# Performance work log

Measured on AMD Instinct MI355X. Metric: run time of the kernel, lower is better.

## Reference

```python
import jax, jax.numpy as jnp
import numpy as np

B, S, HIDDEN = 1, 2048, 2048
NUM_HEADS, MLA_DIM = 16, 128
HEAD_DIM = HIDDEN // NUM_HEADS
ROPE_BASE = 10000.0


def setup_inputs() -> dict:
    key = jax.random.key(0)
    ks = jax.random.split(key, 5)
    sd = 0.02
    hidden_states = jax.random.normal(ks[0], (B, S, HIDDEN), dtype=jnp.float32)
    wq = jax.random.normal(ks[1], (HIDDEN, NUM_HEADS * MLA_DIM), dtype=jnp.float32) * sd
    wk = jax.random.normal(ks[2], (HIDDEN, NUM_HEADS * MLA_DIM), dtype=jnp.float32) * sd
    wv = jax.random.normal(ks[3], (HIDDEN, HIDDEN), dtype=jnp.float32) * sd
    wo = jax.random.normal(ks[4], (HIDDEN, HIDDEN), dtype=jnp.float32) * sd
    # causal additive mask [B, 1, S, S]
    causal = jnp.tril(jnp.ones((S, S), dtype=bool))
    attention_mask = jnp.where(causal, 0.0, -1e9).astype(jnp.float32)[None, None]
    attention_mask = jnp.broadcast_to(attention_mask, (B, 1, S, S))
    return {"hidden_states": hidden_states, "wq": wq, "wk": wk, "wv": wv,
            "wo": wo, "attention_mask": attention_mask}


def _rope_cos_sin(seq_len, dim, dtype):
    inv_freq = 1.0 / (ROPE_BASE ** (jnp.arange(0, dim, 2, dtype=jnp.float32) / dim))
    t = jnp.arange(seq_len, dtype=jnp.float32)
    freqs = jnp.einsum('i,j->ij', t, inv_freq)           # [S, dim/2]
    emb = jnp.concatenate([freqs, freqs], axis=-1)       # [S, dim]
    cos = jnp.cos(emb)[None, :, None, :].astype(dtype)   # [1, S, 1, dim]
    sin = jnp.sin(emb)[None, :, None, :].astype(dtype)
    return cos, sin


def _rotate_half(x):
    x1, x2 = jnp.split(x, 2, axis=-1)
    return jnp.concatenate([-x2, x1], axis=-1)


def reference(hidden_states, wq, wk, wv, wo, attention_mask):
    b, s, _ = hidden_states.shape
    q = (hidden_states @ wq).reshape(b, s, NUM_HEADS, MLA_DIM)
    k = (hidden_states @ wk).reshape(b, s, NUM_HEADS, MLA_DIM)
    v = (hidden_states @ wv).reshape(b, s, NUM_HEADS, HEAD_DIM)
    cos, sin = _rope_cos_sin(s, MLA_DIM, q.dtype)
    q = q * cos + _rotate_half(q) * sin
    k = k * cos + _rotate_half(k) * sin
    scale = 1.0 / np.sqrt(MLA_DIM)
    scores = jnp.einsum('bqhd,bkhd->bhqk', q, k) * scale + attention_mask
    probs = jax.nn.softmax(scores, axis=-1)
    out = jnp.einsum('bhqk,bkhd->bqhd', probs, v).reshape(b, s, HIDDEN)
    return out @ wo
```

## Files before the change

kernel.cpp:

```cpp
#include <hip/hip_runtime.h>
#include <math.h>

namespace {

constexpr int SEQ = 2048;
constexpr int HID = 2048;
constexpr int NH  = 16;
constexpr int DH  = 128;

using f32x4  = __attribute__((ext_vector_type(4))) float;
using short8 = __attribute__((ext_vector_type(8))) short;

__device__ __forceinline__ unsigned short f2bf(float f) {
    unsigned u = __float_as_uint(f);
    u += 0x7FFFu + ((u >> 16) & 1u);
    return (unsigned short)(u >> 16);
}

typedef const __attribute__((address_space(1))) unsigned int GUI;
typedef __attribute__((address_space(3))) unsigned int LUI;
__device__ __forceinline__ void async16(const void* g, void* l) {
    __builtin_amdgcn_global_load_lds((GUI*)g, (LUI*)l, 16, 0, 0);
}

__global__ __launch_bounds__(256)
void cast_bf16(const float* __restrict__ X, unsigned short* __restrict__ Y)
{
    const int i = blockIdx.x * 256 + threadIdx.x;
    const float4 v = reinterpret_cast<const float4*>(X)[i];
    ushort4 o;
    o.x = f2bf(v.x); o.y = f2bf(v.y); o.z = f2bf(v.z); o.w = f2bf(v.w);
    reinterpret_cast<ushort4*>(Y)[i] = o;
}

__global__ __launch_bounds__(256)
void transpose_cast3(const float* __restrict__ w0, const float* __restrict__ w1,
                     const float* __restrict__ w2, unsigned short* __restrict__ WT3)
{
    const int z = blockIdx.z;
    const float* W = (z == 0) ? w0 : (z == 1) ? w1 : w2;
    unsigned short* WT = WT3 + (size_t)z * HID * HID;

    __shared__ float t[32][66];
    const int tx = threadIdx.x & 31, ty = threadIdx.x >> 5;
    const int n0 = blockIdx.x * 64, k0 = blockIdx.y * 32;
    #pragma unroll
    for (int i = 0; i < 4; ++i) {
        const int kr = ty + 8 * i;
        const float2 v = *reinterpret_cast<const float2*>(
            &W[(size_t)(k0 + kr) * HID + n0 + 2 * tx]);
        t[kr][2 * tx]     = v.x;
        t[kr][2 * tx + 1] = v.y;
    }
    __syncthreads();
    #pragma unroll
    for (int i = 0; i < 8; ++i) {
        const int n = ty + 8 * i;
        WT[(size_t)(n0 + n) * HID + k0 + tx] = f2bf(t[tx][n]);
    }
}

__global__ __launch_bounds__(256)
void transpose_cast(const float* __restrict__ W, unsigned short* __restrict__ WT)
{
    __shared__ float t[32][66];
    const int tx = threadIdx.x & 31, ty = threadIdx.x >> 5;
    const int n0 = blockIdx.x * 64, k0 = blockIdx.y * 32;
    #pragma unroll
    for (int i = 0; i < 4; ++i) {
        const int kr = ty + 8 * i;
        const float2 v = *reinterpret_cast<const float2*>(
            &W[(size_t)(k0 + kr) * HID + n0 + 2 * tx]);
        t[kr][2 * tx]     = v.x;
        t[kr][2 * tx + 1] = v.y;
    }
    __syncthreads();
    #pragma unroll
    for (int i = 0; i < 8; ++i) {
        const int n = ty + 8 * i;
        WT[(size_t)(n0 + n) * HID + k0 + tx] = f2bf(t[tx][n]);
    }
}

__global__ __launch_bounds__(256)
void transp_bf16(const unsigned short* __restrict__ X, unsigned short* __restrict__ Y)
{
    __shared__ unsigned short t[32][34];
    const int tx = threadIdx.x & 31, ty = threadIdx.x >> 5;
    const int i0 = blockIdx.y * 32, j0 = blockIdx.x * 32;
    #pragma unroll
    for (int q = 0; q < 4; ++q)
        t[ty + 8 * q][tx] = X[(size_t)(i0 + ty + 8 * q) * HID + j0 + tx];
    __syncthreads();
    #pragma unroll
    for (int q = 0; q < 4; ++q)
        Y[(size_t)(j0 + ty + 8 * q) * HID + i0 + tx] = t[tx][ty + 8 * q];
}

__global__ __launch_bounds__(256)
void gemm_qkv(const unsigned short* __restrict__ A,
              const unsigned short* __restrict__ Bt3,
              unsigned short* __restrict__ Qo,
              unsigned short* __restrict__ Ko,
              unsigned short* __restrict__ Vo)
{
    __shared__ unsigned short As[128 * 32];
    __shared__ unsigned short Bs[128 * 32];

    const int tid  = threadIdx.x;
    const int lane = tid & 63;
    const int w    = tid >> 6;
    const int wr   = w >> 1, wc = w & 1;

    const int b  = blockIdx.x;
    const int sw = (b & 7) * 96 + (b >> 3);
    const int mt = sw & 15, nt = sw >> 4;
    const int m0  = mt * 128;
    const int n0g = nt * 128;
    const int wi  = nt >> 4;
    const int n0  = (nt & 15) * 128;
    unsigned short* C = (wi == 0) ? Qo : (wi == 1) ? Ko : Vo;

    const int srow = lane >> 2;
    const int scol = (lane & 3) * 8;
    const int c0   = w * 2;

    const unsigned short* gA = A   + (size_t)(m0  + c0 * 16 + srow) * HID + scol;
    const unsigned short* gB = Bt3 + (size_t)(n0g + c0 * 16 + srow) * HID + scol;
    unsigned short* lA = &As[c0 * 16 * 32];
    unsigned short* lB = &Bs[c0 * 16 * 32];

    f32x4 acc[4][4] = {};

    for (int k0 = 0; k0 < HID; k0 += 32) {
        __syncthreads();
        async16(gA + k0,            lA);
        async16(gA + 16 * HID + k0, lA + 16 * 32);
        async16(gB + k0,            lB);
        async16(gB + 16 * HID + k0, lB + 16 * 32);
        __syncthreads();

        short8 af[4], bf[4];
        const int kb = (lane >> 4) * 8;
        #pragma unroll
        for (int i = 0; i < 4; ++i) {
            af[i] = *reinterpret_cast<const short8*>(
                &As[(wr * 64 + i * 16 + (lane & 15)) * 32 + kb]);
            bf[i] = *reinterpret_cast<const short8*>(
                &Bs[(wc * 64 + i * 16 + (lane & 15)) * 32 + kb]);
        }
        #pragma unroll
        for (int i = 0; i < 4; ++i)
            #pragma unroll
            for (int j = 0; j < 4; ++j)
                acc[i][j] = __builtin_amdgcn_mfma_f32_16x16x32_bf16(
                    af[i], bf[j], acc[i][j], 0, 0, 0);
    }

    const int cl = lane & 15, rg = (lane >> 4) * 4;
    #pragma unroll
    for (int i = 0; i < 4; ++i)
        #pragma unroll
        for (int j = 0; j < 4; ++j)
            #pragma unroll
            for (int rr = 0; rr < 4; ++rr) {
                const int row = m0 + wr * 64 + i * 16 + rg + rr;
                const int col = n0 + wc * 64 + j * 16 + cl;
                C[(size_t)row * HID + col] = f2bf(acc[i][j][rr]);
            }
}

__global__ __launch_bounds__(256)
void gemm_wo_sk(const unsigned short* __restrict__ A,
                const unsigned short* __restrict__ Bt,
                float* __restrict__ P0, float* __restrict__ P1)
{
    __shared__ unsigned short As[128 * 32];
    __shared__ unsigned short Bs[128 * 32];

    const int tid  = threadIdx.x;
    const int lane = tid & 63;
    const int w    = tid >> 6;
    const int wr   = w >> 1, wc = w & 1;

    const int b     = blockIdx.x;
    const int chunk = b >> 8;
    const int bb    = b & 255;
    const int sw = (bb & 7) * 32 + (bb >> 3);
    const int m0 = (sw >> 4) * 128, n0 = (sw & 15) * 128;
    float* C = chunk ? P1 : P0;
    const int kbase = chunk * 1024;

    const int srow = lane >> 2;
    const int scol = (lane & 3) * 8;
    const int c0   = w * 2;

    const unsigned short* gA = A  + (size_t)(m0 + c0 * 16 + srow) * HID + kbase + scol;
    const unsigned short* gB = Bt + (size_t)(n0 + c0 * 16 + srow) * HID + kbase + scol;
    unsigned short* lA = &As[c0 * 16 * 32];
    unsigned short* lB = &Bs[c0 * 16 * 32];

    f32x4 acc[4][4] = {};

    for (int k0 = 0; k0 < 1024; k0 += 32) {
        __syncthreads();
        async16(gA + k0,            lA);
        async16(gA + 16 * HID + k0, lA + 16 * 32);
        async16(gB + k0,            lB);
        async16(gB + 16 * HID + k0, lB + 16 * 32);
        __syncthreads();

        short8 af[4], bf[4];
        const int kb = (lane >> 4) * 8;
        #pragma unroll
        for (int i = 0; i < 4; ++i) {
            af[i] = *reinterpret_cast<const short8*>(
                &As[(wr * 64 + i * 16 + (lane & 15)) * 32 + kb]);
            bf[i] = *reinterpret_cast<const short8*>(
                &Bs[(wc * 64 + i * 16 + (lane & 15)) * 32 + kb]);
        }
        #pragma unroll
        for (int i = 0; i < 4; ++i)
            #pragma unroll
            for (int j = 0; j < 4; ++j)
                acc[i][j] = __builtin_amdgcn_mfma_f32_16x16x32_bf16(
                    af[i], bf[j], acc[i][j], 0, 0, 0);
    }

    const int cl = lane & 15, rg = (lane >> 4) * 4;
    #pragma unroll
    for (int i = 0; i < 4; ++i)
        #pragma unroll
        for (int j = 0; j < 4; ++j)
            #pragma unroll
            for (int rr = 0; rr < 4; ++rr) {
                const int row = m0 + wr * 64 + i * 16 + rg + rr;
                const int col = n0 + wc * 64 + j * 16 + cl;
                C[(size_t)row * HID + col] = acc[i][j][rr];
            }
}

__global__ __launch_bounds__(256)
void reduce2(const float* __restrict__ P0, const float* __restrict__ P1,
             float* __restrict__ out)
{
    const int i = blockIdx.x * 256 + threadIdx.x;
    const float4 a = reinterpret_cast<const float4*>(P0)[i];
    const float4 b = reinterpret_cast<const float4*>(P1)[i];
    float4 r; r.x = a.x + b.x; r.y = a.y + b.y; r.z = a.z + b.z; r.w = a.w + b.w;
    reinterpret_cast<float4*>(out)[i] = r;
}

__global__ __launch_bounds__(256)
void rope_qk(unsigned short* __restrict__ Q, unsigned short* __restrict__ K)
{
    const int idx = blockIdx.x * 256 + threadIdx.x;
    const int d = idx & 63;
    const int h = (idx >> 6) & (NH - 1);
    const int s = idx >> 10;

    const float invf = exp2f(-(float)d * (13.287712379549449f / 64.0f));
    float sn, c;
    sincosf((float)s * invf, &sn, &c);

    const float SC = 0.08838834764831845f;
    const size_t base = (size_t)s * HID + h * DH + d;

    const float a0 = __uint_as_float((unsigned)Q[base]      << 16);
    const float a1 = __uint_as_float((unsigned)Q[base + 64] << 16);
    Q[base]      = f2bf((a0 * c - a1 * sn) * SC);
    Q[base + 64] = f2bf((a1 * c + a0 * sn) * SC);
    const float b0 = __uint_as_float((unsigned)K[base]      << 16);
    const float b1 = __uint_as_float((unsigned)K[base + 64] << 16);
    K[base]      = f2bf(b0 * c - b1 * sn);
    K[base + 64] = f2bf(b1 * c + b0 * sn);
}

__global__ __launch_bounds__(256)
void attn_mfma(const unsigned short* __restrict__ Q,
               const unsigned short* __restrict__ K,
               const unsigned short* __restrict__ Vt,
               unsigned short* __restrict__ AO)
{
    __shared__ unsigned short Ks[2][64 * 128];
    __shared__ unsigned short Vs[2][128 * 64];
    __shared__ unsigned short Ps[4][16 * 72];

    const int tid  = threadIdx.x;
    const int lane = tid & 63;
    const int w    = tid >> 6;

    const int b  = blockIdx.x;
    const int i_ = b & 31;
    const int h  = b >> 5;
    const int qb = (b < 256) ? i_ : 31 - i_;
    const int q0 = qb * 64;

    const int cl = lane & 15;
    const int lg = lane >> 4;
    const int rg = lg * 4;

    short8 aq[4];
    const unsigned short* qrow = Q + (size_t)(q0 + w * 16 + cl) * HID + h * DH;
    #pragma unroll
    for (int c = 0; c < 4; ++c)
        aq[c] = *reinterpret_cast<const short8*>(qrow + c * 32 + lg * 8);

    f32x4 o[8] = {};
    float m[4] = {-INFINITY, -INFINITY, -INFINITY, -INFINITY};
    float l[4] = {};

    auto stage = [&](int t, int buf) {
        const int k0 = t * 64;
        #pragma unroll
        for (int i = 0; i < 4; ++i) {
            const int rb = i * 16 + w * 4;
            const int r  = rb + lg;
            const int gs = cl ^ (r & 7);
            async16(K + (size_t)(k0 + r) * HID + h * DH + gs * 8,
                    &Ks[buf][rb * 128]);
        }
        #pragma unroll
        for (int i = 0; i < 4; ++i) {
            const int rb = i * 32 + w * 8;
            const int r  = rb + (lane >> 3);
            const int gs = (lane & 7) ^ (r & 7);
            async16(Vt + (size_t)(h * DH + r) * SEQ + k0 + gs * 8,
                    &Vs[buf][rb * 64]);
        }
    };

    const int nt = qb + 1;
    stage(0, 0);

    for (int t = 0; t < nt; ++t) {
        const int cur = t & 1;
        __syncthreads();
        if (t + 1 < nt) stage(t + 1, cur ^ 1);

        f32x4 s4[4] = {};
        #pragma unroll
        for (int jk = 0; jk < 4; ++jk) {
            #pragma unroll
            for (int c = 0; c < 4; ++c) {
                const int row  = jk * 16 + cl;
                const int slot = (c * 4 + lg) ^ (row & 7);
                const short8 bk = *reinterpret_cast<const short8*>(
                    &Ks[cur][row * 128 + slot * 8]);
                s4[jk] = __builtin_amdgcn_mfma_f32_16x16x32_bf16(
                    aq[c], bk, s4[jk], 0, 0, 0);
            }
        }

        if (t == nt - 1) {
            #pragma unroll
            for (int jk = 0; jk < 4; ++jk)
                #pragma unroll
                for (int r = 0; r < 4; ++r)
                    if (jk * 16 + cl > w * 16 + rg + r)
                        s4[jk][r] = -INFINITY;
        }

        float corr[4], rs[4];
        #pragma unroll
        for (int r = 0; r < 4; ++r) {
            float mx = fmaxf(fmaxf(s4[0][r], s4[1][r]),
                             fmaxf(s4[2][r], s4[3][r]));
            #pragma unroll
            for (int off = 1; off < 16; off <<= 1)
                mx = fmaxf(mx, __shfl_xor(mx, off, 64));
            const float mn = fmaxf(m[r], mx);
            corr[r] = __expf(m[r] - mn);
            m[r] = mn;
            rs[r] = 0.0f;
        }
        #pragma unroll
        for (int jk = 0; jk < 4; ++jk)
            #pragma unroll
            for (int r = 0; r < 4; ++r) {
                const float p = __expf(s4[jk][r] - m[r]);
                Ps[w][(rg + r) * 72 + jk * 16 + cl] = f2bf(p);
                rs[r] += p;
            }
        #pragma unroll
        for (int r = 0; r < 4; ++r) {
            #pragma unroll
            for (int off = 1; off < 16; off <<= 1)
                rs[r] += __shfl_xor(rs[r], off, 64);
            l[r] = l[r] * corr[r] + rs[r];
        }
        #pragma unroll
        for (int jd = 0; jd < 8; ++jd)
            #pragma unroll
            for (int r = 0; r < 4; ++r)
                o[jd][r] *= corr[r];

        #pragma unroll
        for (int c = 0; c < 2; ++c) {
            const short8 pa = *reinterpret_cast<const short8*>(
                &Ps[w][cl * 72 + c * 32 + lg * 8]);
            #pragma unroll
            for (int jd = 0; jd < 8; ++jd) {
                const int row  = jd * 16 + cl;
                const int slot = (c * 4 + lg) ^ (row & 7);
                const short8 bv = *reinterpret_cast<const short8*>(
                    &Vs[cur][row * 64 + slot * 8]);
                o[jd] = __builtin_amdgcn_mfma_f32_16x16x32_bf16(
                    pa, bv, o[jd], 0, 0, 0);
            }
        }
    }

    #pragma unroll
    for (int r = 0; r < 4; ++r) {
        const float inv = 1.0f / l[r];
        unsigned short* orow = AO + (size_t)(q0 + w * 16 + rg + r) * HID + h * DH;
        #pragma unroll
        for (int jd = 0; jd < 8; ++jd)
            orow[jd * 16 + cl] = f2bf(o[jd][r] * inv);
    }
}

}

extern "C" void kernel_launch(void* const* d_in, const int* in_sizes, int n_in,
                              void* d_out, int out_size, void* d_ws, size_t ws_size,
                              hipStream_t stream)
{
    (void)in_sizes; (void)n_in; (void)out_size; (void)ws_size;

    const float* hs = (const float*)d_in[0];
    const float* wq = (const float*)d_in[1];
    const float* wk = (const float*)d_in[2];
    const float* wv = (const float*)d_in[3];
    const float* wo = (const float*)d_in[4];
    float* out = (float*)d_out;

    const size_t NE = (size_t)SEQ * HID;
    unsigned short* hsb = (unsigned short*)d_ws;
    unsigned short* Qb  = hsb + NE;
    unsigned short* Kb  = Qb + NE;
    unsigned short* Vb  = Kb + NE;
    unsigned short* WT3 = Vb + NE;
    unsigned short* AOb = WT3 + NE;
    unsigned short* WTo = WT3;
    unsigned short* Vt  = hsb;
    float* P0 = (float*)hsb;
    float* P1 = (float*)Kb;

    cast_bf16<<<(NE / 4) / 256, 256, 0, stream>>>(hs, hsb);

    transpose_cast3<<<dim3(HID / 64, HID / 32, 3), 256, 0, stream>>>(wq, wk, wv, WT3);

    gemm_qkv<<<768, 256, 0, stream>>>(hsb, WT3, Qb, Kb, Vb);

    rope_qk<<<(SEQ * NH * 64) / 256, 256, 0, stream>>>(Qb, Kb);

    transp_bf16<<<dim3(HID / 32, HID / 32), 256, 0, stream>>>(Vb, Vt);

    attn_mfma<<<512, 256, 0, stream>>>(Qb, Kb, Vt, AOb);

    transpose_cast<<<dim3(HID / 64, HID / 32), 256, 0, stream>>>(wo, WTo);
    gemm_wo_sk<<<512, 256, 0, stream>>>(AOb, WTo, P0, P1);
    reduce2<<<(int)(NE / 4 / 256), 256, 0, stream>>>(P0, P1, out);
}
```

Before: 313.1 us.

## Split causal attention over key range with partial outputs and a combine kernel

Splits each long causal query block's key range into two halves handled by separate workgroups (768 instead of 512), writing unnormalized partial outputs plus per-row max and sum, then merges them in a new combine kernel. The aim is better load balance and CU utilisation across the causal triangle. It also drops the double-buffered K/V staging in favour of a single buffer with two barriers per tile, and raises wave priority around the MFMA sections. Costs are the extra partial-output traffic, a second launch, and losing copy/compute overlap inside the attention loop.

```diff
diff --git a/kernel.cpp b/kernel.cpp
--- a/kernel.cpp
+++ b/kernel.cpp
@@ -11,6 +11,8 @@
 using f32x4  = __attribute__((ext_vector_type(4))) float;
 using short8 = __attribute__((ext_vector_type(8))) short;
 
+__device__ __forceinline__ float bflo(unsigned u) { return __uint_as_float(u << 16); }
+__device__ __forceinline__ float bfhi(unsigned u) { return __uint_as_float(u & 0xFFFF0000u); }
 __device__ __forceinline__ unsigned short f2bf(float f) {
     unsigned u = __float_as_uint(f);
     u += 0x7FFFu + ((u >> 16) & 1u);
@@ -277,23 +279,41 @@
 }
 
 __global__ __launch_bounds__(256)
-void attn_mfma(const unsigned short* __restrict__ Q,
+void attn_part(const unsigned short* __restrict__ Q,
                const unsigned short* __restrict__ K,
                const unsigned short* __restrict__ Vt,
-               unsigned short* __restrict__ AO)
-{
-    __shared__ unsigned short Ks[2][64 * 128];
-    __shared__ unsigned short Vs[2][128 * 64];
+               unsigned short* __restrict__ O1, unsigned short* __restrict__ O2,
+               float2* __restrict__ ML1, float2* __restrict__ ML2)
+{
+    __shared__ unsigned short Ks[64 * 128];
+    __shared__ unsigned short Vs[128 * 64];
     __shared__ unsigned short Ps[4][16 * 72];
 
     const int tid  = threadIdx.x;
     const int lane = tid & 63;
     const int w    = tid >> 6;
 
-    const int b  = blockIdx.x;
-    const int i_ = b & 31;
-    const int h  = b >> 5;
-    const int qb = (b < 256) ? i_ : 31 - i_;
+    int h, qb, t0, t1, pidx;
+    unsigned short* Op;
+    float2* MLp;
+    const int b = blockIdx.x;
+    if (b < 256) {
+        h = b >> 4; qb = 16 + (b & 15);
+        t0 = 0; t1 = 16;
+        pidx = h * 32 + qb; Op = O1; MLp = ML1;
+    } else {
+        const int idx = b - 256;
+        const int wr_ = idx >> 5;
+        const int wi_ = idx & 31;
+        h = wi_ >> 1;
+        if ((wi_ & 1) == 0) {
+            qb = 15 - wr_; t0 = 0; t1 = qb + 1;
+            pidx = h * 32 + qb; Op = O1; MLp = ML1;
+        } else {
+            qb = 31 - wr_; t0 = 16; t1 = qb + 1;
+            pidx = h * 16 + (qb - 16); Op = O2; MLp = ML2;
+        }
+    }
     const int q0 = qb * 64;
 
     const int cl = lane & 15;
@@ -310,35 +330,28 @@
     float m[4] = {-INFINITY, -INFINITY, -INFINITY, -INFINITY};
     float l[4] = {};
 
-    auto stage = [&](int t, int buf) {
+    for (int t = t0; t < t1; ++t) {
         const int k0 = t * 64;
+
+        __syncthreads();
         #pragma unroll
         for (int i = 0; i < 4; ++i) {
             const int rb = i * 16 + w * 4;
             const int r  = rb + lg;
             const int gs = cl ^ (r & 7);
-            async16(K + (size_t)(k0 + r) * HID + h * DH + gs * 8,
-                    &Ks[buf][rb * 128]);
+            async16(K + (size_t)(k0 + r) * HID + h * DH + gs * 8, &Ks[rb * 128]);
         }
         #pragma unroll
         for (int i = 0; i < 4; ++i) {
             const int rb = i * 32 + w * 8;
             const int r  = rb + (lane >> 3);
             const int gs = (lane & 7) ^ (r & 7);
-            async16(Vt + (size_t)(h * DH + r) * SEQ + k0 + gs * 8,
-                    &Vs[buf][rb * 64]);
-        }
-    };
-
-    const int nt = qb + 1;
-    stage(0, 0);
-
-    for (int t = 0; t < nt; ++t) {
-        const int cur = t & 1;
+            async16(Vt + (size_t)(h * DH + r) * SEQ + k0 + gs * 8, &Vs[rb * 64]);
+        }
         __syncthreads();
-        if (t + 1 < nt) stage(t + 1, cur ^ 1);
 
         f32x4 s4[4] = {};
+        __builtin_amdgcn_s_setprio(1);
         #pragma unroll
         for (int jk = 0; jk < 4; ++jk) {
             #pragma unroll
@@ -346,13 +359,14 @@
                 const int row  = jk * 16 + cl;
                 const int slot = (c * 4 + lg) ^ (row & 7);
                 const short8 bk = *reinterpret_cast<const short8*>(
-                    &Ks[cur][row * 128 + slot * 8]);
+                    &Ks[row * 128 + slot * 8]);
                 s4[jk] = __builtin_amdgcn_mfma_f32_16x16x32_bf16(
                     aq[c], bk, s4[jk], 0, 0, 0);
             }
         }
-
-        if (t == nt - 1) {
+        __builtin_amdgcn_s_setprio(0);
+
+        if (t == qb) {
             #pragma unroll
             for (int jk = 0; jk < 4; ++jk)
                 #pragma unroll
@@ -395,6 +409,7 @@
             for (int r = 0; r < 4; ++r)
                 o[jd][r] *= corr[r];
 
+        __builtin_amdgcn_s_setprio(1);
         #pragma unroll
         for (int c = 0; c < 2; ++c) {
             const short8 pa = *reinterpret_cast<const short8*>(
@@ -404,21 +419,60 @@
                 const int row  = jd * 16 + cl;
                 const int slot = (c * 4 + lg) ^ (row & 7);
                 const short8 bv = *reinterpret_cast<const short8*>(
-                    &Vs[cur][row * 64 + slot * 8]);
+                    &Vs[row * 64 + slot * 8]);
                 o[jd] = __builtin_amdgcn_mfma_f32_16x16x32_bf16(
                     pa, bv, o[jd], 0, 0, 0);
             }
         }
+        __builtin_amdgcn_s_setprio(0);
     }
 
     #pragma unroll
     for (int r = 0; r < 4; ++r) {
-        const float inv = 1.0f / l[r];
-        unsigned short* orow = AO + (size_t)(q0 + w * 16 + rg + r) * HID + h * DH;
+        const int row = w * 16 + rg + r;
+        if (cl == 0)
+            MLp[(size_t)pidx * 64 + row] = make_float2(m[r], l[r]);
+        unsigned short* orow = Op + ((size_t)pidx * 64 + row) * DH;
         #pragma unroll
         for (int jd = 0; jd < 8; ++jd)
-            orow[jd * 16 + cl] = f2bf(o[jd][r] * inv);
-    }
+            orow[jd * 16 + cl] = f2bf(o[jd][r]);
+    }
+}
+
+__global__ __launch_bounds__(256)
+void attn_combine(const unsigned short* __restrict__ O1,
+                  const unsigned short* __restrict__ O2,
+                  const float2* __restrict__ ML1,
+                  const float2* __restrict__ ML2,
+                  unsigned short* __restrict__ AO)
+{
+    const int idx = blockIdx.x * 256 + threadIdx.x;
+    const int dp  = idx & 63;
+    const int row = (idx >> 6) & 63;
+    const int qb  = (idx >> 12) & 31;
+    const int h   = idx >> 17;
+
+    const int p1 = h * 32 + qb;
+    const float2 ml1 = ML1[(size_t)p1 * 64 + row];
+    const unsigned u1 = reinterpret_cast<const unsigned*>(O1)[((size_t)p1 * 64 + row) * 64 + dp];
+    float o0 = bflo(u1), o1v = bfhi(u1);
+    float L = ml1.y;
+
+    if (qb >= 16) {
+        const int p2 = h * 16 + (qb - 16);
+        const float2 ml2 = ML2[(size_t)p2 * 64 + row];
+        const unsigned u2 = reinterpret_cast<const unsigned*>(O2)[((size_t)p2 * 64 + row) * 64 + dp];
+        const float M  = fmaxf(ml1.x, ml2.x);
+        const float e1 = __expf(ml1.x - M);
+        const float e2 = __expf(ml2.x - M);
+        o0  = o0  * e1 + bflo(u2) * e2;
+        o1v = o1v * e1 + bfhi(u2) * e2;
+        L   = ml1.y * e1 + ml2.y * e2;
+    }
+
+    const float inv = 1.0f / L;
+    const unsigned out = (unsigned)f2bf(o0 * inv) | ((unsigned)f2bf(o1v * inv) << 16);
+    reinterpret_cast<unsigned*>(AO)[((size_t)(qb * 64 + row) * HID + h * DH) / 2 + dp] = out;
 }
 
 }
@@ -442,7 +496,11 @@
     unsigned short* Kb  = Qb + NE;
     unsigned short* Vb  = Kb + NE;
     unsigned short* WT3 = Vb + NE;
+    unsigned short* O1  = WT3;
     unsigned short* AOb = WT3 + NE;
+    unsigned short* O2  = WT3 + 2 * NE;
+    float2* ML1 = (float2*)(O2 + 2 * 1024 * 1024);
+    float2* ML2 = ML1 + 16 * 32 * 64;
     unsigned short* WTo = WT3;
     unsigned short* Vt  = hsb;
     float* P0 = (float*)hsb;
@@ -458,7 +516,8 @@
 
     transp_bf16<<<dim3(HID / 32, HID / 32), 256, 0, stream>>>(Vb, Vt);
 
-    attn_mfma<<<512, 256, 0, stream>>>(Qb, Kb, Vt, AOb);
+    attn_part<<<768, 256, 0, stream>>>(Qb, Kb, Vt, O1, O2, ML1, ML2);
+    attn_combine<<<8192, 256, 0, stream>>>(O1, O2, ML1, ML2, AOb);
 
     transpose_cast<<<dim3(HID / 64, HID / 32), 256, 0, stream>>>(wo, WTo);
     gemm_wo_sk<<<512, 256, 0, stream>>>(AOb, WTo, P0, P1);
```

Result: faster. 303.8 us (-3.0%).
